# Kernel tuning notes

Hardware: AMD Instinct MI355X
Metric: run time of the kernel (lower is better)

Reference implementation:

```python
import jax, jax.numpy as jnp
import numpy as np

SCALE = 768.0  # scale = output_features


def setup_inputs() -> dict:
    key = jax.random.key(0)
    k1, k2, k3, k4 = jax.random.split(key, 4)
    B, S, D, F = 8, 2048, 768, 768
    x = jax.random.normal(k1, (B, S, D), dtype=jnp.float32)
    # torch nn.Linear weights: shape (out_features, in_features), y = x @ W.T
    Wq = jax.random.normal(k2, (F, D), dtype=jnp.float32) * (1.0 / np.sqrt(D))
    Wk = jax.random.normal(k3, (F, D), dtype=jnp.float32) * (1.0 / np.sqrt(D))
    Wv = jax.random.normal(k4, (F, D), dtype=jnp.float32) * (1.0 / np.sqrt(D))
    return {"x": x, "Wq": Wq, "Wk": Wk, "Wv": Wv}


def _cdist_l2(q, k):
    # pairwise Euclidean distances, [B, S, S]; matches torch.cdist(q, k, p=2)
    q2 = jnp.sum(q * q, axis=-1)  # [B, S]
    k2 = jnp.sum(k * k, axis=-1)  # [B, S]
    qk = jnp.einsum('bid,bjd->bij', q, k)  # [B, S, S]
    d2 = q2[:, :, None] + k2[:, None, :] - 2.0 * qk
    return jnp.sqrt(jnp.maximum(d2, 0.0))


def reference(x, Wq, Wk, Wv):
    q = jnp.einsum('bsd,fd->bsf', x, Wq)
    k = jnp.einsum('bsd,fd->bsf', x, Wk)
    v = jnp.einsum('bsd,fd->bsf', x, Wv)
    scores = _cdist_l2(q, k) / jnp.sqrt(jnp.asarray(SCALE, dtype=x.dtype))
    attn = jax.nn.softmax(scores, axis=-1)  # NOTE: source softmaxes raw distances (no negation)
    return jnp.einsum('bij,bjf->bif', attn, v)
```

## Files before the change

kernel.cpp:

```cpp
#include <hip/hip_runtime.h>
#include <hip/hip_fp8.h>
#include <stdint.h>
#include <math.h>


typedef __attribute__((ext_vector_type(8))) __bf16 bf16x8;
typedef __attribute__((ext_vector_type(4))) float f32x4;
typedef __attribute__((ext_vector_type(4))) unsigned int u32x4;
typedef __attribute__((ext_vector_type(2))) unsigned int u32x2;

__device__ __forceinline__ unsigned short f2b(float f) {
    unsigned u = __float_as_uint(f);
    unsigned r = 0x7fffu + ((u >> 16) & 1u);
    return (unsigned short)((u + r) >> 16);
}
__device__ __forceinline__ float b2f(unsigned short h) {
    return __uint_as_float(((unsigned)h) << 16);
}
__device__ __forceinline__ unsigned char f2f8(float f) {
    __hip_fp8_e4m3 t(f);
    return t.__x;
}
__device__ __forceinline__ float f8tof(unsigned char b) {
    int e = (b >> 3) & 15, m = b & 7;
    float v = e ? ldexpf(8.0f + m, e - 10) : ldexpf((float)m, -9);
    return (b & 0x80) ? -v : v;
}

__device__ __forceinline__ void wg_barrier() {
    asm volatile("" ::: "memory");
    __builtin_amdgcn_s_barrier();
    asm volatile("" ::: "memory");
}

__device__ __forceinline__ unsigned lds_off(const void* p) {
    return (unsigned)(uintptr_t)(const __attribute__((address_space(3))) char*)p;
}

__global__ __launch_bounds__(256) void castk(const float* __restrict__ src,
                                             unsigned short* __restrict__ dst, int n4) {
    int i = blockIdx.x * 256 + threadIdx.x;
    if (i >= n4) return;
    float4 v = ((const float4*)src)[i];
    ushort4 o;
    o.x = f2b(v.x); o.y = f2b(v.y); o.z = f2b(v.z); o.w = f2b(v.w);
    ((ushort4*)dst)[i] = o;
}

__global__ __launch_bounds__(256) void rowreduce8(const unsigned char* __restrict__ X,
                                                  int L, int rows, float* __restrict__ out) {
    int w = threadIdx.x >> 6, lane = threadIdx.x & 63;
    int row = blockIdx.x * 4 + w;
    if (row >= rows) return;
    const unsigned char* xr = X + (size_t)row * L;
    float s = 0.f;
    int passes = L >> 8;
    for (int p = 0; p < passes; ++p) {
        uchar4 u = *(const uchar4*)(xr + (p << 8) + lane * 4);
        float a = f8tof(u.x), b = f8tof(u.y), c = f8tof(u.z), d = f8tof(u.w);
        s += a * a + b * b + c * c + d * d;
    }
#pragma unroll
    for (int o = 32; o > 0; o >>= 1) s += __shfl_down(s, o);
    if (lane == 0) out[row] = s;
}

#define MF(A_, B_, C_) (C_) = __builtin_amdgcn_mfma_f32_16x16x32_bf16((A_), (B_), (C_), 0, 0, 0)
#define MF8(A_, B_, C_) (C_) = __builtin_amdgcn_mfma_f32_16x16x32_fp8_fp8((A_), (B_), (C_), 0, 0, 0)
#define DSR(dst_, a_, imm_) \
    asm volatile("ds_read_b128 %0, %1 offset:" #imm_ : "=v"(dst_) : "v"(a_))
#define DSR64(dst_, a_, imm_) \
    asm volatile("ds_read_b64 %0, %1 offset:" #imm_ : "=v"(dst_) : "v"(a_))
#define GL4(d_, p_) asm volatile("global_load_dwordx4 %0, %1, off" : "=v"(d_) : "v"(p_))
#define GL2(d_, p_) asm volatile("global_load_dwordx2 %0, %1, off" : "=v"(d_) : "v"(p_))
#define DSW(a_, imm_, d_) \
    asm volatile("ds_write_b128 %0, %1 offset:" #imm_ :: "v"(a_), "v"(d_) : "memory")
#define DSW64(a_, imm_, d_) \
    asm volatile("ds_write_b64 %0, %1 offset:" #imm_ :: "v"(a_), "v"(d_) : "memory")
#define LGKM(n_) asm volatile("s_waitcnt lgkmcnt(" #n_ ")" ::: "memory")
#define VMC0 asm volatile("s_waitcnt vmcnt(0)" ::: "memory")
#define SB0 __builtin_amdgcn_sched_barrier(0)

#define LOADT(T_) do {                                                     \
    const size_t ko_ = (size_t)(T_) * 64;                                  \
    GL4(ra0, pa + ko_);             GL4(ra1, pa + lda64 + ko_);            \
    GL4(ra2, pa + 2 * lda64 + ko_); GL4(ra3, pa + 3 * lda64 + ko_);        \
    GL4(rb0, pb + ko_);             GL4(rb1, pb + ldb64 + ko_);            \
    GL4(rb2, pb + 2 * ldb64 + ko_); GL4(rb3, pb + 3 * ldb64 + ko_);        \
} while (0)
#define WRITET(WB_) do {                                                   \
    const unsigned wa_ = wA + (WB_), wb2_ = wB + (WB_);                    \
    DSW(wa_, 0, ra0);     DSW(wa_, 8192, ra1);                             \
    DSW(wa_, 16384, ra2); DSW(wa_, 24576, ra3);                            \
    DSW(wb2_, 0, rb0);     DSW(wb2_, 8192, rb1);                           \
    DSW(wb2_, 16384, rb2); DSW(wb2_, 24576, rb3);                          \
} while (0)

template <int EPI>
__global__ __launch_bounds__(512, 2) void gemm256(
    const unsigned short* __restrict__ A, int lda, long long sA,
    const unsigned short* __restrict__ B, int ldb, long long sB,
    void* __restrict__ Cv, int ldc, long long sC,
    int Kd, int perm,
    const float* __restrict__ aux1, int sAux1) {
    __shared__ __attribute__((aligned(128))) unsigned short As[2 * 256 * 64];
    __shared__ __attribute__((aligned(128))) unsigned short Bs[2 * 256 * 64];

    const int z = perm ? blockIdx.x : blockIdx.z;
    const int jb = perm ? blockIdx.y : blockIdx.x;
    const int ib = perm ? blockIdx.z : blockIdx.y;
    const unsigned short* __restrict__ Ab = A + (size_t)z * sA;
    const unsigned short* __restrict__ Bb = B + (size_t)z * sB;
    const int i0 = ib * 256, j0 = jb * 256;
    const int tid = threadIdx.x;
    const int w = tid >> 6, lane = tid & 63;
    const int wr = w >> 2, wc = w & 3;
    const int c16 = lane & 15, kq = lane >> 4;

    const int lr0 = tid >> 3;
    const int clog0 = (tid & 7) ^ (lr0 & 7);
    const unsigned short* pa = Ab + (size_t)(i0 + lr0) * lda + clog0 * 8;
    const unsigned short* pb = Bb + (size_t)(j0 + lr0) * ldb + clog0 * 8;
    const size_t lda64 = (size_t)64 * lda, ldb64 = (size_t)64 * ldb;

    const unsigned wA = lds_off(As) + (unsigned)tid * 16;
    const unsigned wB = lds_off(Bs) + (unsigned)tid * 16;

    const int swc = (kq ^ (c16 & 7)) << 4;
    const unsigned adrA0 = lds_off(As) + (unsigned)(wr * 128 + c16) * 128 + swc;
    const unsigned adrA0x = adrA0 ^ 64u;
    const unsigned adrB0 = lds_off(Bs) + (unsigned)(wc * 64 + c16) * 128 + swc;
    const unsigned adrB0x = adrB0 ^ 64u;

    f32x4 acc[8][4];
    const f32x4 zero = {0.f, 0.f, 0.f, 0.f};
#pragma unroll
    for (int i = 0; i < 8; ++i)
#pragma unroll
        for (int j = 0; j < 4; ++j) acc[i][j] = zero;

    u32x4 ra0, ra1, ra2, ra3, rb0, rb1, rb2, rb3;
    bf16x8 aL[4][2], aH[4][2], bF[4][2];

    const int nt = Kd >> 6;

    LOADT(0);
    VMC0;
    WRITET(0u);
    LOADT(1);
    LGKM(0);
    wg_barrier();

    for (int t = 0; t < nt; ++t) {
        const unsigned rb_ = (t & 1) ? 32768u : 0u;
        const unsigned wb_ = (t & 1) ? 0u : 32768u;
        const unsigned aA = adrA0 + rb_, aAx = adrA0x + rb_;
        const unsigned aB = adrB0 + rb_, aBx = adrB0x + rb_;
        DSR(aL[0][0], aA, 0);    DSR(aL[0][1], aAx, 0);
        DSR(aL[1][0], aA, 2048); DSR(aL[1][1], aAx, 2048);
        DSR(aL[2][0], aA, 4096); DSR(aL[2][1], aAx, 4096);
        DSR(aL[3][0], aA, 6144); DSR(aL[3][1], aAx, 6144);
        DSR(bF[0][0], aB, 0);    DSR(bF[0][1], aBx, 0);
        DSR(bF[1][0], aB, 2048); DSR(bF[1][1], aBx, 2048);
        DSR(bF[2][0], aB, 4096); DSR(bF[2][1], aBx, 4096);
        DSR(bF[3][0], aB, 6144); DSR(bF[3][1], aBx, 6144);
        if (t + 1 < nt) {
            VMC0;
            WRITET(wb_);
            if (t + 2 < nt) LOADT(t + 2);
            LGKM(8);
        } else {
            LGKM(0);
        }
        SB0;
        __builtin_amdgcn_s_setprio(1);
#pragma unroll
        for (int kk = 0; kk < 2; ++kk)
#pragma unroll
            for (int mi = 0; mi < 4; ++mi)
#pragma unroll
                for (int ni = 0; ni < 4; ++ni)
                    MF(aL[mi][kk], bF[ni][kk], acc[mi][ni]);
        __builtin_amdgcn_s_setprio(0);
        DSR(aH[0][0], aA, 8192);  DSR(aH[0][1], aAx, 8192);
        DSR(aH[1][0], aA, 10240); DSR(aH[1][1], aAx, 10240);
        DSR(aH[2][0], aA, 12288); DSR(aH[2][1], aAx, 12288);
        DSR(aH[3][0], aA, 14336); DSR(aH[3][1], aAx, 14336);
        LGKM(0); SB0;
        __builtin_amdgcn_s_setprio(1);
#pragma unroll
        for (int kk = 0; kk < 2; ++kk)
#pragma unroll
            for (int mi = 0; mi < 4; ++mi)
#pragma unroll
                for (int ni = 0; ni < 4; ++ni)
                    MF(aH[mi][kk], bF[ni][kk], acc[4 + mi][ni]);
        __builtin_amdgcn_s_setprio(0);
        wg_barrier();
    }
    const int prow = kq * 4;
    if constexpr (EPI == 0) {
        unsigned short* C = (unsigned short*)Cv + (size_t)z * sC;
        unsigned short* sc = (unsigned short*)((char*)As + w * 8192);
        const int rr = lane >> 3, ch = lane & 7;
#pragma unroll
        for (int mi = 0; mi < 8; ++mi) {
#pragma unroll
            for (int ni = 0; ni < 4; ++ni)
#pragma unroll
                for (int r = 0; r < 4; ++r)
                    sc[(prow + r) * 72 + ni * 16 + c16] = f2b(acc[mi][ni][r]);
#pragma unroll
            for (int pass = 0; pass < 2; ++pass) {
                const int r2 = rr + 8 * pass;
                bf16x8 v = *(const bf16x8*)&sc[r2 * 72 + ch * 8];
                const int grow = i0 + wr * 128 + mi * 16 + r2;
                *(bf16x8*)&C[(size_t)grow * ldc + j0 + wc * 64 + ch * 8] = v;
            }
        }
    } else if constexpr (EPI == 3) {
        unsigned char* C = (unsigned char*)Cv + (size_t)z * sC;
        unsigned char* sc = (unsigned char*)As + w * 8192;
        const int rr = lane >> 2, ch = lane & 3;
#pragma unroll
        for (int mi = 0; mi < 8; ++mi) {
#pragma unroll
            for (int ni = 0; ni < 4; ++ni)
#pragma unroll
                for (int r = 0; r < 4; ++r)
                    sc[(prow + r) * 80 + ni * 16 + c16] = f2f8(acc[mi][ni][r]);
            u32x4 v = *(const u32x4*)&sc[rr * 80 + ch * 16];
            const int grow = i0 + wr * 128 + mi * 16 + rr;
            *(u32x4*)&C[(size_t)grow * ldc + j0 + wc * 64 + ch * 16] = v;
        }
    } else {
        float* C = (float*)Cv + (size_t)z * sC;
        const float* lp = aux1 + (size_t)z * 8 * 2048;
        float* sc = (float*)((char*)As + w * 8192);
        const int rr = lane >> 4, ch = lane & 15;
#pragma unroll
        for (int mi = 0; mi < 8; ++mi) {
            float linv[4];
#pragma unroll
            for (int r = 0; r < 4; ++r) {
                const int grow = i0 + wr * 128 + mi * 16 + prow + r;
                float s = 0.f;
#pragma unroll
                for (int j = 0; j < 8; ++j) s += lp[j * 2048 + grow];
                linv[r] = 1.0f / s;
            }
#pragma unroll
            for (int ni = 0; ni < 4; ++ni)
#pragma unroll
                for (int r = 0; r < 4; ++r)
                    sc[(prow + r) * 68 + ni * 16 + c16] = acc[mi][ni][r] * linv[r];
#pragma unroll
            for (int pass = 0; pass < 4; ++pass) {
                const int r2 = rr + 4 * pass;
                f32x4 v = *(const f32x4*)&sc[r2 * 68 + ch * 4];
                const int grow = i0 + wr * 128 + mi * 16 + r2;
                *(f32x4*)&C[(size_t)grow * ldc + j0 + wc * 64 + ch * 4] = v;
            }
        }
    }
}

#define LOADT8(T_) do {                                                    \
    const size_t ko_ = (size_t)(T_) * 64;                                  \
    GL2(fa0, pa8 + ko_);              GL2(fa1, pa8 + lda64b + ko_);        \
    GL2(fa2, pa8 + 2 * lda64b + ko_); GL2(fa3, pa8 + 3 * lda64b + ko_);    \
    GL2(fb0, pb8 + ko_);              GL2(fb1, pb8 + ldb64b + ko_);        \
    GL2(fb2, pb8 + 2 * ldb64b + ko_); GL2(fb3, pb8 + 3 * ldb64b + ko_);    \
} while (0)
#define WRITET8(WB_) do {                                                  \
    const unsigned wa_ = wA8 + (WB_), wb2_ = wB8 + (WB_);                  \
    DSW64(wa_, 0, fa0);     DSW64(wa_, 4096, fa1);                         \
    DSW64(wa_, 8192, fa2);  DSW64(wa_, 12288, fa3);                        \
    DSW64(wb2_, 0, fb0);    DSW64(wb2_, 4096, fb1);                        \
    DSW64(wb2_, 8192, fb2); DSW64(wb2_, 12288, fb3);                       \
} while (0)

__global__ __launch_bounds__(512, 2) void gemm256f8(
    const unsigned char* __restrict__ A, int lda, long long sA,
    const unsigned char* __restrict__ B, int ldb, long long sB,
    unsigned short* __restrict__ Cq, int ldc, long long sC,
    int Kd,
    const float* __restrict__ q2a, int sQ2,
    const float* __restrict__ k2a, int sK2,
    float* __restrict__ lpart, float invs) {
    __shared__ __attribute__((aligned(128))) unsigned char As8[2 * 256 * 64];
    __shared__ __attribute__((aligned(128))) unsigned char Bs8[2 * 256 * 64];

    const int z = blockIdx.x;
    const int jb = blockIdx.y, ib = blockIdx.z;
    const unsigned char* __restrict__ Ab = A + (size_t)z * sA;
    const unsigned char* __restrict__ Bb = B + (size_t)z * sB;
    const int i0 = ib * 256, j0 = jb * 256;
    const int tid = threadIdx.x;
    const int w = tid >> 6, lane = tid & 63;
    const int wr = w >> 2, wc = w & 3;
    const int c16 = lane & 15, kq = lane >> 4;

    const int lr0 = tid >> 3;
    const int slog = (tid & 7) ^ (lr0 & 7);
    const unsigned char* pa8 = Ab + (size_t)(i0 + lr0) * lda + slog * 8;
    const unsigned char* pb8 = Bb + (size_t)(j0 + lr0) * ldb + slog * 8;
    const size_t lda64b = (size_t)64 * lda, ldb64b = (size_t)64 * ldb;

    const unsigned wA8 = lds_off(As8) + (unsigned)tid * 8;
    const unsigned wB8 = lds_off(Bs8) + (unsigned)tid * 8;

    const int sw8 = (kq ^ (c16 & 7)) << 3;
    const unsigned adrA0 = lds_off(As8) + (unsigned)(wr * 128 + c16) * 64 + sw8;
    const unsigned adrA0x = adrA0 ^ 32u;
    const unsigned adrB0 = lds_off(Bs8) + (unsigned)(wc * 64 + c16) * 64 + sw8;
    const unsigned adrB0x = adrB0 ^ 32u;

    f32x4 acc[8][4];
    const f32x4 zero = {0.f, 0.f, 0.f, 0.f};
#pragma unroll
    for (int i = 0; i < 8; ++i)
#pragma unroll
        for (int j = 0; j < 4; ++j) acc[i][j] = zero;

    u32x2 fa0, fa1, fa2, fa3, fb0, fb1, fb2, fb3;
    long aL[4][2], aH[4][2], bF[4][2];

    const int nt = Kd >> 6;

    LOADT8(0);
    VMC0;
    WRITET8(0u);
    LOADT8(1);
    LGKM(0);
    wg_barrier();

    for (int t = 0; t < nt; ++t) {
        const unsigned rb_ = (t & 1) ? 16384u : 0u;
        const unsigned wb_ = (t & 1) ? 0u : 16384u;
        const unsigned aA = adrA0 + rb_, aAx = adrA0x + rb_;
        const unsigned aB = adrB0 + rb_, aBx = adrB0x + rb_;
        DSR64(aL[0][0], aA, 0);    DSR64(aL[0][1], aAx, 0);
        DSR64(aL[1][0], aA, 1024); DSR64(aL[1][1], aAx, 1024);
        DSR64(aL[2][0], aA, 2048); DSR64(aL[2][1], aAx, 2048);
        DSR64(aL[3][0], aA, 3072); DSR64(aL[3][1], aAx, 3072);
        DSR64(bF[0][0], aB, 0);    DSR64(bF[0][1], aBx, 0);
        DSR64(bF[1][0], aB, 1024); DSR64(bF[1][1], aBx, 1024);
        DSR64(bF[2][0], aB, 2048); DSR64(bF[2][1], aBx, 2048);
        DSR64(bF[3][0], aB, 3072); DSR64(bF[3][1], aBx, 3072);
        if (t + 1 < nt) {
            VMC0;
            WRITET8(wb_);
            if (t + 2 < nt) LOADT8(t + 2);
            LGKM(8);
        } else {
            LGKM(0);
        }
        SB0;
        __builtin_amdgcn_s_setprio(1);
#pragma unroll
        for (int kk = 0; kk < 2; ++kk)
#pragma unroll
            for (int mi = 0; mi < 4; ++mi)
#pragma unroll
                for (int ni = 0; ni < 4; ++ni)
                    MF8(aL[mi][kk], bF[ni][kk], acc[mi][ni]);
        __builtin_amdgcn_s_setprio(0);
        DSR64(aH[0][0], aA, 4096); DSR64(aH[0][1], aAx, 4096);
        DSR64(aH[1][0], aA, 5120); DSR64(aH[1][1], aAx, 5120);
        DSR64(aH[2][0], aA, 6144); DSR64(aH[2][1], aAx, 6144);
        DSR64(aH[3][0], aA, 7168); DSR64(aH[3][1], aAx, 7168);
        LGKM(0); SB0;
        __builtin_amdgcn_s_setprio(1);
#pragma unroll
        for (int kk = 0; kk < 2; ++kk)
#pragma unroll
            for (int mi = 0; mi < 4; ++mi)
#pragma unroll
                for (int ni = 0; ni < 4; ++ni)
                    MF8(aH[mi][kk], bF[ni][kk], acc[4 + mi][ni]);
        __builtin_amdgcn_s_setprio(0);
        wg_barrier();
    }

    unsigned short* C = Cq + (size_t)z * sC;
    const float* q2b = q2a + (size_t)z * sQ2;
    const float* k2b = k2a + (size_t)z * sK2;
    unsigned short* sc = (unsigned short*)(As8 + w * 4096);
    float* lred = (float*)Bs8;
    const int prow = kq * 4;
    const int rr = lane >> 3, ch = lane & 7;
#pragma unroll
    for (int mi = 0; mi < 8; ++mi) {
        float ev[4][4];
#pragma unroll
        for (int ni = 0; ni < 4; ++ni) {
            const int col = j0 + wc * 64 + ni * 16 + c16;
            const float k2v = k2b[col];
#pragma unroll
            for (int r = 0; r < 4; ++r) {
                const int grow = i0 + wr * 128 + mi * 16 + prow + r;
                float d2 = q2b[grow] + k2v - 2.0f * acc[mi][ni][r];
                ev[ni][r] = __expf(sqrtf(fmaxf(d2, 0.f)) * invs);
            }
        }
#pragma unroll
        for (int r = 0; r < 4; ++r) {
            float s = ev[0][r] + ev[1][r] + ev[2][r] + ev[3][r];
#pragma unroll
            for (int m = 1; m < 16; m <<= 1) s += __shfl_xor(s, m);
            if (c16 == 0)
                lred[(wr * 4 + wc) * 128 + mi * 16 + prow + r] = s;
        }
#pragma unroll
        for (int ni = 0; ni < 4; ++ni)
#pragma unroll
            for (int r = 0; r < 4; ++r)
                sc[(prow + r) * 72 + ni * 16 + c16] = f2b(ev[ni][r]);
#pragma unroll
        for (int pass = 0; pass < 2; ++pass) {
            const int r2 = rr + 8 * pass;
            bf16x8 v = *(const bf16x8*)&sc[r2 * 72 + ch * 8];
            const int grow = i0 + wr * 128 + mi * 16 + r2;
            *(bf16x8*)&C[(size_t)grow * ldc + j0 + wc * 64 + ch * 8] = v;
        }
    }
    LGKM(0);
    wg_barrier();
    if (wc == 0) {
        float* lrow = lpart + ((size_t)z * 8 + jb) * 2048 + i0 + wr * 128;
#pragma unroll
        for (int h = 0; h < 2; ++h) {
            const int row = lane + h * 64;
            float s = lred[(wr * 4 + 0) * 128 + row] + lred[(wr * 4 + 1) * 128 + row] +
                      lred[(wr * 4 + 2) * 128 + row] + lred[(wr * 4 + 3) * 128 + row];
            lrow[row] = s;
        }
    }
}

extern "C" void kernel_launch(void* const* d_in, const int* in_sizes, int n_in,
                              void* d_out, int out_size, void* d_ws, size_t ws_size,
                              hipStream_t stream) {
    const float* x = (const float*)d_in[0];
    const float* Wq = (const float*)d_in[1];
    const float* Wk = (const float*)d_in[2];
    const float* Wv = (const float*)d_in[3];
    const int Bz = 8, S = 2048, D = 768, F = 768;
    const int BS = Bz * S;

    const size_t szX = (size_t)BS * D * 2;
    const size_t szW = (size_t)F * D * 2;
    const size_t szQ8 = (size_t)BS * F;
    const size_t szE = (size_t)Bz * S * S * 2;

    char* p = (char*)d_ws;
    unsigned short* xb = (unsigned short*)p;  p += szX;
    unsigned short* Wqb = (unsigned short*)p; p += szW;
    unsigned short* Wkb = (unsigned short*)p; p += szW;
    unsigned short* Wvb = (unsigned short*)p; p += szW;
    unsigned char* Q8 = (unsigned char*)p;    p += szQ8;
    unsigned char* K8 = (unsigned char*)p;    p += szQ8;
    unsigned short* VT = (unsigned short*)p;  p += szX;
    unsigned short* E = (unsigned short*)p;   p += szE;
    float* q2 = (float*)p;    p += (size_t)BS * 4;
    float* k2 = (float*)p;    p += (size_t)BS * 4;
    float* lpart = (float*)p; p += (size_t)Bz * 8 * 2048 * 4;
    if ((size_t)(p - (char*)d_ws) > ws_size) return;

    const float invs = 1.0f / sqrtf(768.0f);

    castk<<<(BS * D / 4 + 255) / 256, 256, 0, stream>>>(x, xb, BS * D / 4);
    castk<<<(F * D / 4 + 255) / 256, 256, 0, stream>>>(Wq, Wqb, F * D / 4);
    castk<<<(F * D / 4 + 255) / 256, 256, 0, stream>>>(Wk, Wkb, F * D / 4);
    castk<<<(F * D / 4 + 255) / 256, 256, 0, stream>>>(Wv, Wvb, F * D / 4);

    gemm256<3><<<dim3(F / 256, BS / 256, 2), 512, 0, stream>>>(
        xb, D, 0,
        Wqb, D, (long long)F * D,
        Q8, F, (long long)BS * F,
        D, 0, nullptr, 0);

    gemm256<0><<<dim3(BS / 256, F / 256, 1), 512, 0, stream>>>(
        Wvb, D, 0,
        xb, D, 0,
        VT, BS, 0,
        D, 0, nullptr, 0);

    rowreduce8<<<BS / 4, 256, 0, stream>>>(Q8, F, BS, q2);
    rowreduce8<<<BS / 4, 256, 0, stream>>>(K8, F, BS, k2);

    gemm256f8<<<dim3(Bz, S / 256, S / 256), 512, 0, stream>>>(
        Q8, F, (long long)S * F,
        K8, F, (long long)S * F,
        E, S, (long long)S * S,
        F, q2, S, k2, S, lpart, invs);

    gemm256<2><<<dim3(Bz, F / 256, S / 256), 512, 0, stream>>>(
        E, S, (long long)S * S,
        VT, BS, (long long)S,
        d_out, F, (long long)S * F,
        S, 1, lpart, 0);
}
```

Measured before the change: 241.7 us.

## Compute softmax row sums from bf16 E tiles inside the PV GEMM

Removes the row-sum reduction (shuffles, LDS staging, lpart global writes) from the QK/exp epilogue. The PV GEMM instead accumulates row sums from the bf16 A fragments it already loads, with one warp column summing low halves and another high halves, then reduces through LDS before normalising. This drops a workspace buffer and its reads, but adds VALU work inside the PV main loop for half the waves. It also makes the denominator use the rounded bf16 values, which matches the numerator more consistently.

Measured after the change: 261.2 us. +8.1%, slower.

```diff
diff --git a/kernel.cpp b/kernel.cpp
--- a/kernel.cpp
+++ b/kernel.cpp
@@ -35,6 +35,15 @@
 
 __device__ __forceinline__ unsigned lds_off(const void* p) {
     return (unsigned)(uintptr_t)(const __attribute__((address_space(3))) char*)p;
+}
+
+__device__ __forceinline__ void acc8(float& s, const bf16x8& v) {
+    u32x4 u = __builtin_bit_cast(u32x4, v);
+#pragma unroll
+    for (int i = 0; i < 4; ++i) {
+        s += __uint_as_float(u[i] << 16);
+        s += __uint_as_float(u[i] & 0xffff0000u);
+    }
 }
 
 __global__ __launch_bounds__(256) void castk(const float* __restrict__ src,
@@ -138,6 +147,8 @@
     for (int i = 0; i < 8; ++i)
 #pragma unroll
         for (int j = 0; j < 4; ++j) acc[i][j] = zero;
+
+    float lacc[4] = {0.f, 0.f, 0.f, 0.f};
 
     u32x4 ra0, ra1, ra2, ra3, rb0, rb1, rb2, rb3;
     bf16x8 aL[4][2], aH[4][2], bF[4][2];
@@ -182,6 +193,15 @@
                 for (int ni = 0; ni < 4; ++ni)
                     MF(aL[mi][kk], bF[ni][kk], acc[mi][ni]);
         __builtin_amdgcn_s_setprio(0);
+        if constexpr (EPI == 2) {
+            if (wc == 0) {
+#pragma unroll
+                for (int mi = 0; mi < 4; ++mi) {
+                    acc8(lacc[mi], aL[mi][0]);
+                    acc8(lacc[mi], aL[mi][1]);
+                }
+            }
+        }
         DSR(aH[0][0], aA, 8192);  DSR(aH[0][1], aAx, 8192);
         DSR(aH[1][0], aA, 10240); DSR(aH[1][1], aAx, 10240);
         DSR(aH[2][0], aA, 12288); DSR(aH[2][1], aAx, 12288);
@@ -196,8 +216,18 @@
                 for (int ni = 0; ni < 4; ++ni)
                     MF(aH[mi][kk], bF[ni][kk], acc[4 + mi][ni]);
         __builtin_amdgcn_s_setprio(0);
+        if constexpr (EPI == 2) {
+            if (wc == 1) {
+#pragma unroll
+                for (int mi = 0; mi < 4; ++mi) {
+                    acc8(lacc[mi], aH[mi][0]);
+                    acc8(lacc[mi], aH[mi][1]);
+                }
+            }
+        }
         wg_barrier();
     }
+
     const int prow = kq * 4;
     if constexpr (EPI == 0) {
         unsigned short* C = (unsigned short*)Cv + (size_t)z * sC;
@@ -234,21 +264,26 @@
             *(u32x4*)&C[(size_t)grow * ldc + j0 + wc * 64 + ch * 16] = v;
         }
     } else {
+        float* ls = (float*)Bs;
+        if (wc < 2) {
+#pragma unroll
+            for (int mi = 0; mi < 4; ++mi) {
+                float s = lacc[mi];
+                s += __shfl_xor(s, 16);
+                s += __shfl_xor(s, 32);
+                if (kq == 0) ls[wr * 128 + wc * 64 + mi * 16 + c16] = s;
+            }
+        }
+        __syncthreads();
         float* C = (float*)Cv + (size_t)z * sC;
-        const float* lp = aux1 + (size_t)z * 8 * 2048;
         float* sc = (float*)((char*)As + w * 8192);
         const int rr = lane >> 4, ch = lane & 15;
 #pragma unroll
         for (int mi = 0; mi < 8; ++mi) {
             float linv[4];
 #pragma unroll
-            for (int r = 0; r < 4; ++r) {
-                const int grow = i0 + wr * 128 + mi * 16 + prow + r;
-                float s = 0.f;
-#pragma unroll
-                for (int j = 0; j < 8; ++j) s += lp[j * 2048 + grow];
-                linv[r] = 1.0f / s;
-            }
+            for (int r = 0; r < 4; ++r)
+                linv[r] = 1.0f / ls[wr * 128 + mi * 16 + prow + r];
 #pragma unroll
             for (int ni = 0; ni < 4; ++ni)
 #pragma unroll
@@ -287,7 +322,7 @@
     int Kd,
     const float* __restrict__ q2a, int sQ2,
     const float* __restrict__ k2a, int sK2,
-    float* __restrict__ lpart, float invs) {
+    float invs) {
     __shared__ __attribute__((aligned(128))) unsigned char As8[2 * 256 * 64];
     __shared__ __attribute__((aligned(128))) unsigned char Bs8[2 * 256 * 64];
 
@@ -387,12 +422,10 @@
     const float* q2b = q2a + (size_t)z * sQ2;
     const float* k2b = k2a + (size_t)z * sK2;
     unsigned short* sc = (unsigned short*)(As8 + w * 4096);
-    float* lred = (float*)Bs8;
     const int prow = kq * 4;
     const int rr = lane >> 3, ch = lane & 7;
 #pragma unroll
     for (int mi = 0; mi < 8; ++mi) {
-        float ev[4][4];
 #pragma unroll
         for (int ni = 0; ni < 4; ++ni) {
             const int col = j0 + wc * 64 + ni * 16 + c16;
@@ -401,40 +434,16 @@
             for (int r = 0; r < 4; ++r) {
                 const int grow = i0 + wr * 128 + mi * 16 + prow + r;
                 float d2 = q2b[grow] + k2v - 2.0f * acc[mi][ni][r];
-                ev[ni][r] = __expf(sqrtf(fmaxf(d2, 0.f)) * invs);
+                float e = __expf(sqrtf(fmaxf(d2, 0.f)) * invs);
+                sc[(prow + r) * 72 + ni * 16 + c16] = f2b(e);
             }
         }
-#pragma unroll
-        for (int r = 0; r < 4; ++r) {
-            float s = ev[0][r] + ev[1][r] + ev[2][r] + ev[3][r];
-#pragma unroll
-            for (int m = 1; m < 16; m <<= 1) s += __shfl_xor(s, m);
-            if (c16 == 0)
-                lred[(wr * 4 + wc) * 128 + mi * 16 + prow + r] = s;
-        }
-#pragma unroll
-        for (int ni = 0; ni < 4; ++ni)
-#pragma unroll
-            for (int r = 0; r < 4; ++r)
-                sc[(prow + r) * 72 + ni * 16 + c16] = f2b(ev[ni][r]);
 #pragma unroll
         for (int pass = 0; pass < 2; ++pass) {
             const int r2 = rr + 8 * pass;
             bf16x8 v = *(const bf16x8*)&sc[r2 * 72 + ch * 8];
             const int grow = i0 + wr * 128 + mi * 16 + r2;
             *(bf16x8*)&C[(size_t)grow * ldc + j0 + wc * 64 + ch * 8] = v;
-        }
-    }
-    LGKM(0);
-    wg_barrier();
-    if (wc == 0) {
-        float* lrow = lpart + ((size_t)z * 8 + jb) * 2048 + i0 + wr * 128;
-#pragma unroll
-        for (int h = 0; h < 2; ++h) {
-            const int row = lane + h * 64;
-            float s = lred[(wr * 4 + 0) * 128 + row] + lred[(wr * 4 + 1) * 128 + row] +
-                      lred[(wr * 4 + 2) * 128 + row] + lred[(wr * 4 + 3) * 128 + row];
-            lrow[row] = s;
         }
     }
 }
@@ -465,7 +474,6 @@
     unsigned short* E = (unsigned short*)p;   p += szE;
     float* q2 = (float*)p;    p += (size_t)BS * 4;
     float* k2 = (float*)p;    p += (size_t)BS * 4;
-    float* lpart = (float*)p; p += (size_t)Bz * 8 * 2048 * 4;
     if ((size_t)(p - (char*)d_ws) > ws_size) return;
 
     const float invs = 1.0f / sqrtf(768.0f);
@@ -494,11 +502,11 @@
         Q8, F, (long long)S * F,
         K8, F, (long long)S * F,
         E, S, (long long)S * S,
-        F, q2, S, k2, S, lpart, invs);
+        F, q2, S, k2, S, invs);
 
     gemm256<2><<<dim3(Bz, F / 256, S / 256), 512, 0, stream>>>(
         E, S, (long long)S * S,
         VT, BS, (long long)S,
         d_out, F, (long long)S * F,
-        S, 1, lpart, 0);
-}
+        S, 1, nullptr, 0);
+}
```
